# Kernel optimization log

Measured on AMD Instinct MI355X. Metric: run time of the kernel, lower is better.

The kernel has to match this reference:

```python
import jax, jax.numpy as jnp
import numpy as np

N = 100_000      # num nodes
R = 7            # num relations
D = 64           # input_dim == output_dim
E = 1_600_000    # num edges
EDIM = 16        # edge_input_dim


def setup_inputs() -> dict:
    key = jax.random.key(0)
    ks = jax.random.split(key, 10)
    node_in = jax.random.randint(ks[0], (E,), 0, N)
    node_out = jax.random.randint(ks[1], (E,), 0, N)
    relation = jax.random.randint(ks[2], (E,), 0, R)
    edge_list = jnp.stack([node_in, node_out, relation], axis=1)  # (E, 3)
    x = jax.random.normal(ks[3], (N, D), dtype=jnp.float32)
    edge_weight = jax.random.uniform(ks[4], (E,), dtype=jnp.float32)
    edge_feature = jax.random.normal(ks[5], (E, EDIM), dtype=jnp.float32)
    s = 1.0 / np.sqrt(R * D)
    W_lin = jax.random.uniform(ks[6], (D, R * D), minval=-s, maxval=s, dtype=jnp.float32)
    b_lin = jnp.zeros((D,), jnp.float32)
    s2 = 1.0 / np.sqrt(D)
    W_self = jax.random.uniform(ks[7], (D, D), minval=-s2, maxval=s2, dtype=jnp.float32)
    b_self = jnp.zeros((D,), jnp.float32)
    s3 = 1.0 / np.sqrt(EDIM)
    W_edge = jax.random.uniform(ks[8], (D, EDIM), minval=-s3, maxval=s3, dtype=jnp.float32)
    b_edge = jnp.zeros((D,), jnp.float32)
    return {"x": x, "edge_list": edge_list, "edge_weight": edge_weight,
            "edge_feature": edge_feature, "W_lin": W_lin, "b_lin": b_lin,
            "W_self": W_self, "b_self": b_self, "W_edge": W_edge, "b_edge": b_edge}


def reference(x, edge_list, edge_weight, edge_feature, W_lin, b_lin, W_self, b_self, W_edge, b_edge):
    node_in, node_out, relation = edge_list[:, 0], edge_list[:, 1], edge_list[:, 2]
    # destination index in the flattened (node, relation) space
    seg = node_out * R + relation  # (E,)
    # sparse.mm(adj.T, x): scatter w * x[src] into (N*R, D)
    msg = edge_weight[:, None] * x[node_in]  # (E, D)
    update = jax.ops.segment_sum(msg, seg, num_segments=N * R)  # (N*R, D)
    # edge feature branch: edge_linear then weighted scatter_add
    edge_msg = (edge_feature @ W_edge.T + b_edge) * edge_weight[:, None]  # (E, D)
    update = update + jax.ops.segment_sum(edge_msg, seg, num_segments=N * R)
    update = update.reshape(N, R * D)
    out = update @ W_lin.T + b_lin + x @ W_self.T + b_self
    return jax.nn.relu(out)
```

## Files before the change

### kernel.cpp

```cpp
#include <hip/hip_runtime.h>
#include <hip/hip_bf16.h>
#include <hip/hip_fp16.h>

#define N_NODES 100000
#define R_REL   7
#define E_EDGES 1600000
#define EDIM    16
#define KTOT    640
#define CAP     56

typedef __bf16 bf16_t;
typedef bf16_t bf16x8 __attribute__((ext_vector_type(8)));
typedef bf16_t bf16x4 __attribute__((ext_vector_type(4)));
typedef float  f32x4  __attribute__((ext_vector_type(4)));
typedef unsigned long long u64;

#define RFL(v) __builtin_amdgcn_readfirstlane(v)
#define RL(v, l) __builtin_amdgcn_readlane(v, l)


__global__ void k_prep(const float* __restrict__ x,
                       const float* __restrict__ W_lin, const float* __restrict__ W_self,
                       const float* __restrict__ W_edge, const float* __restrict__ b_edge,
                       int* __restrict__ cnt, bf16_t* __restrict__ xb,
                       bf16_t* __restrict__ Bp) {
    int idx = blockIdx.x * 256 + threadIdx.x;
    if (idx < N_NODES) cnt[idx] = 0;
    if (idx < KTOT * 64) {
        int k = idx >> 6;
        int j = idx & 63;
        float v;
        if (k < 448) {
            v = W_lin[j * 448 + k];
        } else if (k < 512) {
            v = W_self[j * 64 + (k - 448)];
        } else if (k < 624) {
            int r = (k - 512) >> 4, kk = (k - 512) & 15;
            float s = 0.f;
            for (int d = 0; d < 64; d++)
                s = fmaf(W_lin[j * 448 + r * 64 + d], W_edge[d * 16 + kk], s);
            v = s;
        } else if (k < 631) {
            int r = k - 624;
            float s = 0.f;
            for (int d = 0; d < 64; d++)
                s = fmaf(W_lin[j * 448 + r * 64 + d], b_edge[d], s);
            v = s;
        } else {
            v = 0.f;
        }
        Bp[((k >> 3) * 64 + j) * 8 + (k & 7)] = (bf16_t)v;
    }
    int base = idx * 4;
    if (base < N_NODES * 64) {
        float4 v = *(const float4*)(x + base);
        bf16x4 o = {(bf16_t)v.x, (bf16_t)v.y, (bf16_t)v.z, (bf16_t)v.w};
        *(bf16x4*)(xb + base) = o;
    }
}


__global__ void k_scatter(const int* __restrict__ el, const float* __restrict__ wgt,
                          int* __restrict__ cnt, u64* __restrict__ recs8) {
    int e = blockIdx.x * 256 + threadIdx.x;
    if (e >= E_EDGES) return;
    int src = el[e * 3], dst = el[e * 3 + 1], rel = el[e * 3 + 2];
    unsigned short wb = __half_as_ushort(__float2half(wgt[e]));
    int slot = atomicAdd(&cnt[dst], 1);
    unsigned u0 = (unsigned)src | ((unsigned)rel << 17) | ((unsigned)(e & 0xFFF) << 20);
    unsigned u1 = (unsigned)(e >> 12) | ((unsigned)wb << 16);
    recs8[(size_t)dst * CAP + slot] = ((u64)u1 << 32) | u0;
}


__global__ __launch_bounds__(256) void k_main(
    const bf16_t* __restrict__ xb, const float* __restrict__ ef,
    const float* __restrict__ b_lin, const float* __restrict__ b_self,
    const int* __restrict__ cnt, const u64* __restrict__ recs8,
    const bf16_t* __restrict__ Bp, float* __restrict__ out)
{
    __shared__ __align__(16) bf16_t A[16 * KTOT];
    const int wave = threadIdx.x >> 6;
    const int lane = threadIdx.x & 63;
    const int lef  = lane & 15;
    const int nodeBase = blockIdx.x * 16;
    const int n0 = nodeBase + wave * 4;

    const int4 m4 = *(const int4*)(cnt + n0);
    u64    rw[4];
    bf16_t sv[4];
#pragma unroll
    for (int i = 0; i < 4; i++) {
        rw[i] = recs8[(size_t)(n0 + i) * CAP + min(lane, CAP - 1)];
        sv[i] = xb[(n0 + i) * 64 + lane];
    }

#pragma unroll
    for (int i = 0; i < 4; i++) {
        const int row = wave * 4 + i;
        bf16_t* Ar = A + row * KTOT;
        Ar[448 + lane] = sv[i];
        if (lane < 9) Ar[631 + lane] = (bf16_t)0.f;

        int m = (i == 0) ? m4.x : (i == 1) ? m4.y : (i == 2) ? m4.z : m4.w;
        m = min(m, CAP);
        const unsigned u0v = (unsigned)rw[i];
        const unsigned u1v = (unsigned)(rw[i] >> 32);
        const int  relv  = (u0v >> 17) & 7;
        const bool valid = lane < m;

        for (int r = 0; r < R_REL; r++) {
            u64 mr = __ballot(valid && (relv == r));
            float a = 0.f, F = 0.f, s = 0.f;
            while (mr) {
                int i0 = __builtin_ctzll(mr); mr &= mr - 1;
                int i1 = i0, i2 = i0, i3 = i0;
                int nb = 1;
                if (mr) { i1 = __builtin_ctzll(mr); mr &= mr - 1; nb = 2;
                    if (mr) { i2 = __builtin_ctzll(mr); mr &= mr - 1; nb = 3;
                        if (mr) { i3 = __builtin_ctzll(mr); mr &= mr - 1; nb = 4; } } }
                unsigned a0 = RL(u0v, i0), a1 = RL(u0v, i1);
                unsigned a2 = RL(u0v, i2), a3 = RL(u0v, i3);
                unsigned b0 = RL(u1v, i0), b1 = RL(u1v, i1);
                unsigned b2 = RL(u1v, i2), b3 = RL(u1v, i3);
                int s0 = a0 & 0x1FFFF, s1 = a1 & 0x1FFFF;
                int s2 = a2 & 0x1FFFF, s3 = a3 & 0x1FFFF;
                int e0 = (a0 >> 20) | ((b0 & 0x1FF) << 12);
                int e1 = (a1 >> 20) | ((b1 & 0x1FF) << 12);
                int e2 = (a2 >> 20) | ((b2 & 0x1FF) << 12);
                int e3 = (a3 >> 20) | ((b3 & 0x1FF) << 12);
                float w0 = __half2float(__ushort_as_half((unsigned short)(b0 >> 16)));
                float w1 = (nb > 1) ? __half2float(__ushort_as_half((unsigned short)(b1 >> 16))) : 0.f;
                float w2 = (nb > 2) ? __half2float(__ushort_as_half((unsigned short)(b2 >> 16))) : 0.f;
                float w3 = (nb > 3) ? __half2float(__ushort_as_half((unsigned short)(b3 >> 16))) : 0.f;
                float xv0 = (float)xb[s0 * 64 + lane];
                float xv1 = (float)xb[s1 * 64 + lane];
                float xv2 = (float)xb[s2 * 64 + lane];
                float xv3 = (float)xb[s3 * 64 + lane];
                float ev0 = ef[e0 * EDIM + lef];
                float ev1 = ef[e1 * EDIM + lef];
                float ev2 = ef[e2 * EDIM + lef];
                float ev3 = ef[e3 * EDIM + lef];
                a = fmaf(w0, xv0, a); F = fmaf(w0, ev0, F); s += w0;
                a = fmaf(w1, xv1, a); F = fmaf(w1, ev1, F); s += w1;
                a = fmaf(w2, xv2, a); F = fmaf(w2, ev2, F); s += w2;
                a = fmaf(w3, xv3, a); F = fmaf(w3, ev3, F); s += w3;
            }
            Ar[r * 64 + lane] = (bf16_t)a;
            if (lane < EDIM) Ar[512 + r * EDIM + lane] = (bf16_t)F;
            if (lane == 0)   Ar[624 + r] = (bf16_t)s;
        }
    }
    __syncthreads();

    const int quad = lane >> 4;
    const int l15  = lane & 15;
    f32x4 c = {0.f, 0.f, 0.f, 0.f};
#pragma unroll
    for (int s2i = 0; s2i < KTOT / 32; s2i++) {
        bf16x8 a = *(const bf16x8*)(A + l15 * KTOT + s2i * 32 + quad * 8);
        bf16x8 b = *(const bf16x8*)(Bp + (((s2i * 4 + quad) * 64) + wave * 16 + l15) * 8);
        c = __builtin_amdgcn_mfma_f32_16x16x32_bf16(a, b, c, 0, 0, 0);
    }
    const int j = wave * 16 + l15;
    const float bias = b_lin[j] + b_self[j];
#pragma unroll
    for (int q = 0; q < 4; q++) {
        const int n = nodeBase + quad * 4 + q;
        float v = c[q] + bias;
        out[n * 64 + j] = v > 0.f ? v : 0.f;
    }
}


extern "C" void kernel_launch(void* const* d_in, const int* in_sizes, int n_in,
                              void* d_out, int out_size, void* d_ws, size_t ws_size,
                              hipStream_t stream) {
    const float* x      = (const float*)d_in[0];
    const int*   el     = (const int*)  d_in[1];
    const float* wgt    = (const float*)d_in[2];
    const float* ef     = (const float*)d_in[3];
    const float* W_lin  = (const float*)d_in[4];
    const float* b_lin  = (const float*)d_in[5];
    const float* W_self = (const float*)d_in[6];
    const float* b_self = (const float*)d_in[7];
    const float* W_edge = (const float*)d_in[8];
    const float* b_edge = (const float*)d_in[9];
    float* out = (float*)d_out;

    u64*    recs8 = (u64*)d_ws;
    int*    cnt   = (int*)(recs8 + (size_t)N_NODES * CAP);
    bf16_t* xb    = (bf16_t*)(cnt + N_NODES);
    bf16_t* Bp    = xb + (size_t)N_NODES * 64;

    k_prep   <<<6250, 256, 0, stream>>>(x, W_lin, W_self, W_edge, b_edge, cnt, xb, Bp);
    k_scatter<<<6250, 256, 0, stream>>>(el, wgt, cnt, recs8);
    k_main   <<<N_NODES / 16, 256, 0, stream>>>(xb, ef, b_lin, b_self,
                                                cnt, recs8, Bp, out);
}
```

Baseline: 413.3 us.

## Fuse prep and scatter kernels, pad LDS rows, and split the gather batches

```diff
diff --git a/kernel.cpp b/kernel.cpp
--- a/kernel.cpp
+++ b/kernel.cpp
@@ -7,6 +7,7 @@
 #define E_EDGES 1600000
 #define EDIM    16
 #define KTOT    640
+#define KSTR    648
 #define CAP     56
 
 typedef __bf16 bf16_t;
@@ -19,16 +20,39 @@
 #define RL(v, l) __builtin_amdgcn_readlane(v, l)
 
 
-__global__ void k_prep(const float* __restrict__ x,
-                       const float* __restrict__ W_lin, const float* __restrict__ W_self,
-                       const float* __restrict__ W_edge, const float* __restrict__ b_edge,
-                       int* __restrict__ cnt, bf16_t* __restrict__ xb,
-                       bf16_t* __restrict__ Bp) {
-    int idx = blockIdx.x * 256 + threadIdx.x;
-    if (idx < N_NODES) cnt[idx] = 0;
-    if (idx < KTOT * 64) {
-        int k = idx >> 6;
-        int j = idx & 63;
+__device__ __forceinline__ void sc1(int e, int src, int dst, int rel, float w,
+                                    int* __restrict__ cnt, u64* __restrict__ recs8) {
+    unsigned wb = __float_as_uint(w) & 0xFFFFFE00u;
+    int slot = atomicAdd(&cnt[dst], 1);
+    unsigned u0 = (unsigned)src | ((unsigned)rel << 17) | ((unsigned)(e & 0xFFF) << 20);
+    unsigned u1 = ((unsigned)e >> 12) | wb;
+    recs8[(size_t)dst * CAP + slot] = ((u64)u1 << 32) | u0;
+}
+
+__global__ __launch_bounds__(256) void k_pre(
+    const float* __restrict__ x, const int* __restrict__ el,
+    const float* __restrict__ wgt,
+    const float* __restrict__ W_lin, const float* __restrict__ W_self,
+    const float* __restrict__ W_edge, const float* __restrict__ b_edge,
+    int* __restrict__ cnt, bf16_t* __restrict__ xb, bf16_t* __restrict__ Bp,
+    u64* __restrict__ recs8)
+{
+    const int t = blockIdx.x * 256 + threadIdx.x;
+
+    if (t < (N_NODES * 64) / 16) {
+        const float4* xp = (const float4*)(x + (size_t)t * 16);
+        float4 v0 = xp[0], v1 = xp[1], v2 = xp[2], v3 = xp[3];
+        bf16x8 o0 = {(bf16_t)v0.x, (bf16_t)v0.y, (bf16_t)v0.z, (bf16_t)v0.w,
+                     (bf16_t)v1.x, (bf16_t)v1.y, (bf16_t)v1.z, (bf16_t)v1.w};
+        bf16x8 o1 = {(bf16_t)v2.x, (bf16_t)v2.y, (bf16_t)v2.z, (bf16_t)v2.w,
+                     (bf16_t)v3.x, (bf16_t)v3.y, (bf16_t)v3.z, (bf16_t)v3.w};
+        *(bf16x8*)(xb + (size_t)t * 16)     = o0;
+        *(bf16x8*)(xb + (size_t)t * 16 + 8) = o1;
+    }
+
+    if (t < KTOT * 64) {
+        int k = t >> 6;
+        int j = t & 63;
         float v;
         if (k < 448) {
             v = W_lin[j * 448 + k];
@@ -36,40 +60,32 @@
             v = W_self[j * 64 + (k - 448)];
         } else if (k < 624) {
             int r = (k - 512) >> 4, kk = (k - 512) & 15;
-            float s = 0.f;
+            float sacc = 0.f;
             for (int d = 0; d < 64; d++)
-                s = fmaf(W_lin[j * 448 + r * 64 + d], W_edge[d * 16 + kk], s);
-            v = s;
+                sacc = fmaf(W_lin[j * 448 + r * 64 + d], W_edge[d * 16 + kk], sacc);
+            v = sacc;
         } else if (k < 631) {
             int r = k - 624;
-            float s = 0.f;
+            float sacc = 0.f;
             for (int d = 0; d < 64; d++)
-                s = fmaf(W_lin[j * 448 + r * 64 + d], b_edge[d], s);
-            v = s;
+                sacc = fmaf(W_lin[j * 448 + r * 64 + d], b_edge[d], sacc);
+            v = sacc;
         } else {
             v = 0.f;
         }
         Bp[((k >> 3) * 64 + j) * 8 + (k & 7)] = (bf16_t)v;
     }
-    int base = idx * 4;
-    if (base < N_NODES * 64) {
-        float4 v = *(const float4*)(x + base);
-        bf16x4 o = {(bf16_t)v.x, (bf16_t)v.y, (bf16_t)v.z, (bf16_t)v.w};
-        *(bf16x4*)(xb + base) = o;
-    }
-}
-
-
-__global__ void k_scatter(const int* __restrict__ el, const float* __restrict__ wgt,
-                          int* __restrict__ cnt, u64* __restrict__ recs8) {
-    int e = blockIdx.x * 256 + threadIdx.x;
-    if (e >= E_EDGES) return;
-    int src = el[e * 3], dst = el[e * 3 + 1], rel = el[e * 3 + 2];
-    unsigned short wb = __half_as_ushort(__float2half(wgt[e]));
-    int slot = atomicAdd(&cnt[dst], 1);
-    unsigned u0 = (unsigned)src | ((unsigned)rel << 17) | ((unsigned)(e & 0xFFF) << 20);
-    unsigned u1 = (unsigned)(e >> 12) | ((unsigned)wb << 16);
-    recs8[(size_t)dst * CAP + slot] = ((u64)u1 << 32) | u0;
+
+    if (t < E_EDGES / 4) {
+        const int4* ep = (const int4*)(el + (size_t)t * 12);
+        int4 q0 = ep[0], q1 = ep[1], q2 = ep[2];
+        float4 w4 = *(const float4*)(wgt + (size_t)t * 4);
+        int e = t * 4;
+        sc1(e + 0, q0.x, q0.y, q0.z, w4.x, cnt, recs8);
+        sc1(e + 1, q0.w, q1.x, q1.y, w4.y, cnt, recs8);
+        sc1(e + 2, q1.z, q1.w, q2.x, w4.z, cnt, recs8);
+        sc1(e + 3, q2.y, q2.z, q2.w, w4.w, cnt, recs8);
+    }
 }
 
 
@@ -79,7 +95,7 @@
     const int* __restrict__ cnt, const u64* __restrict__ recs8,
     const bf16_t* __restrict__ Bp, float* __restrict__ out)
 {
-    __shared__ __align__(16) bf16_t A[16 * KTOT];
+    __shared__ __align__(16) bf16_t A[16 * KSTR];
     const int wave = threadIdx.x >> 6;
     const int lane = threadIdx.x & 63;
     const int lef  = lane & 15;
@@ -98,7 +114,7 @@
 #pragma unroll
     for (int i = 0; i < 4; i++) {
         const int row = wave * 4 + i;
-        bf16_t* Ar = A + row * KTOT;
+        bf16_t* Ar = A + row * KSTR;
         Ar[448 + lane] = sv[i];
         if (lane < 9) Ar[631 + lane] = (bf16_t)0.f;
 
@@ -114,37 +130,40 @@
             float a = 0.f, F = 0.f, s = 0.f;
             while (mr) {
                 int i0 = __builtin_ctzll(mr); mr &= mr - 1;
-                int i1 = i0, i2 = i0, i3 = i0;
-                int nb = 1;
-                if (mr) { i1 = __builtin_ctzll(mr); mr &= mr - 1; nb = 2;
-                    if (mr) { i2 = __builtin_ctzll(mr); mr &= mr - 1; nb = 3;
-                        if (mr) { i3 = __builtin_ctzll(mr); mr &= mr - 1; nb = 4; } } }
-                unsigned a0 = RL(u0v, i0), a1 = RL(u0v, i1);
-                unsigned a2 = RL(u0v, i2), a3 = RL(u0v, i3);
-                unsigned b0 = RL(u1v, i0), b1 = RL(u1v, i1);
-                unsigned b2 = RL(u1v, i2), b3 = RL(u1v, i3);
-                int s0 = a0 & 0x1FFFF, s1 = a1 & 0x1FFFF;
-                int s2 = a2 & 0x1FFFF, s3 = a3 & 0x1FFFF;
+                int i1 = i0; bool two = false, more = false;
+                if (mr) { i1 = __builtin_ctzll(mr); mr &= mr - 1;
+                          two = true; more = (mr != 0); }
+                unsigned a0 = RL(u0v, i0), b0 = RL(u1v, i0);
+                unsigned a1 = RL(u0v, i1), b1 = RL(u1v, i1);
+                int src0 = a0 & 0x1FFFF, src1 = a1 & 0x1FFFF;
                 int e0 = (a0 >> 20) | ((b0 & 0x1FF) << 12);
                 int e1 = (a1 >> 20) | ((b1 & 0x1FF) << 12);
-                int e2 = (a2 >> 20) | ((b2 & 0x1FF) << 12);
-                int e3 = (a3 >> 20) | ((b3 & 0x1FF) << 12);
-                float w0 = __half2float(__ushort_as_half((unsigned short)(b0 >> 16)));
-                float w1 = (nb > 1) ? __half2float(__ushort_as_half((unsigned short)(b1 >> 16))) : 0.f;
-                float w2 = (nb > 2) ? __half2float(__ushort_as_half((unsigned short)(b2 >> 16))) : 0.f;
-                float w3 = (nb > 3) ? __half2float(__ushort_as_half((unsigned short)(b3 >> 16))) : 0.f;
-                float xv0 = (float)xb[s0 * 64 + lane];
-                float xv1 = (float)xb[s1 * 64 + lane];
-                float xv2 = (float)xb[s2 * 64 + lane];
-                float xv3 = (float)xb[s3 * 64 + lane];
+                float w0 = __uint_as_float(b0 & 0xFFFFFE00u);
+                float w1 = two ? __uint_as_float(b1 & 0xFFFFFE00u) : 0.f;
+                float xv0 = (float)xb[src0 * 64 + lane];
+                float xv1 = (float)xb[src1 * 64 + lane];
                 float ev0 = ef[e0 * EDIM + lef];
                 float ev1 = ef[e1 * EDIM + lef];
-                float ev2 = ef[e2 * EDIM + lef];
-                float ev3 = ef[e3 * EDIM + lef];
+                if (more) {
+                    int i2 = __builtin_ctzll(mr); mr &= mr - 1;
+                    int i3 = i2; bool four = false;
+                    if (mr) { i3 = __builtin_ctzll(mr); mr &= mr - 1; four = true; }
+                    unsigned a2 = RL(u0v, i2), b2 = RL(u1v, i2);
+                    unsigned a3 = RL(u0v, i3), b3 = RL(u1v, i3);
+                    int src2 = a2 & 0x1FFFF, src3 = a3 & 0x1FFFF;
+                    int e2 = (a2 >> 20) | ((b2 & 0x1FF) << 12);
+                    int e3 = (a3 >> 20) | ((b3 & 0x1FF) << 12);
+                    float w2 = __uint_as_float(b2 & 0xFFFFFE00u);
+                    float w3 = four ? __uint_as_float(b3 & 0xFFFFFE00u) : 0.f;
+                    float xv2 = (float)xb[src2 * 64 + lane];
+                    float xv3 = (float)xb[src3 * 64 + lane];
+                    float ev2 = ef[e2 * EDIM + lef];
+                    float ev3 = ef[e3 * EDIM + lef];
+                    a = fmaf(w2, xv2, a); F = fmaf(w2, ev2, F); s += w2;
+                    a = fmaf(w3, xv3, a); F = fmaf(w3, ev3, F); s += w3;
+                }
                 a = fmaf(w0, xv0, a); F = fmaf(w0, ev0, F); s += w0;
                 a = fmaf(w1, xv1, a); F = fmaf(w1, ev1, F); s += w1;
-                a = fmaf(w2, xv2, a); F = fmaf(w2, ev2, F); s += w2;
-                a = fmaf(w3, xv3, a); F = fmaf(w3, ev3, F); s += w3;
             }
             Ar[r * 64 + lane] = (bf16_t)a;
             if (lane < EDIM) Ar[512 + r * EDIM + lane] = (bf16_t)F;
@@ -158,7 +177,7 @@
     f32x4 c = {0.f, 0.f, 0.f, 0.f};
 #pragma unroll
     for (int s2i = 0; s2i < KTOT / 32; s2i++) {
-        bf16x8 a = *(const bf16x8*)(A + l15 * KTOT + s2i * 32 + quad * 8);
+        bf16x8 a = *(const bf16x8*)(A + l15 * KSTR + s2i * 32 + quad * 8);
         bf16x8 b = *(const bf16x8*)(Bp + (((s2i * 4 + quad) * 64) + wave * 16 + l15) * 8);
         c = __builtin_amdgcn_mfma_f32_16x16x32_bf16(a, b, c, 0, 0, 0);
     }
@@ -193,8 +212,9 @@
     bf16_t* xb    = (bf16_t*)(cnt + N_NODES);
     bf16_t* Bp    = xb + (size_t)N_NODES * 64;
 
-    k_prep   <<<6250, 256, 0, stream>>>(x, W_lin, W_self, W_edge, b_edge, cnt, xb, Bp);
-    k_scatter<<<6250, 256, 0, stream>>>(el, wgt, cnt, recs8);
-    k_main   <<<N_NODES / 16, 256, 0, stream>>>(xb, ef, b_lin, b_self,
-                                                cnt, recs8, Bp, out);
-}
+    hipMemsetAsync(cnt, 0, N_NODES * sizeof(int), stream);
+    k_pre <<<1563, 256, 0, stream>>>(x, el, wgt, W_lin, W_self, W_edge, b_edge,
+                                     cnt, xb, Bp, recs8);
+    k_main<<<N_NODES / 16, 256, 0, stream>>>(xb, ef, b_lin, b_self,
+                                             cnt, recs8, Bp, out);
+}
```

New measurement: 388.1 us. 1.07x faster.
